# Kernel tuning notes

Hardware: AMD Instinct MI355X
Metric: run time of the kernel (lower is better)

## Reference

```python
import jax, jax.numpy as jnp
import numpy as np

HEADS = 4
DIM_HEAD = 32
DIM = 64
NUM_MEM = 4


def _rmsnorm(t, g, dim):
    # F.normalize(x, dim=1) * g * sqrt(dim)  (eps=1e-12 like torch)
    n = jnp.sqrt(jnp.sum(t * t, axis=1, keepdims=True))
    return t / jnp.maximum(n, 1e-12) * g * (dim ** 0.5)


def setup_inputs() -> dict:
    key = jax.random.key(0)
    ks = jax.random.split(key, 7)
    b, c, H, W, D = 2, DIM, 48, 48, 48
    hidden = HEADS * DIM_HEAD
    x = jax.random.normal(ks[0], (b, c, H, W, D), dtype=jnp.float32)
    g_in = jnp.ones((1, c, 1, 1, 1), dtype=jnp.float32)
    w_qkv = jax.random.normal(ks[1], (hidden * 3, c), dtype=jnp.float32) * 0.02  # 1x1 conv3d
    mem_kv = jax.random.normal(ks[2], (2, HEADS, DIM_HEAD, NUM_MEM), dtype=jnp.float32)
    w_out = jax.random.normal(ks[3], (c, hidden), dtype=jnp.float32) * 0.02
    b_out = jnp.zeros((c,), dtype=jnp.float32)
    g_out = jnp.ones((1, c, 1, 1, 1), dtype=jnp.float32)
    return {"x": x, "g_in": g_in, "w_qkv": w_qkv, "mem_kv": mem_kv,
            "w_out": w_out, "b_out": b_out, "g_out": g_out}


def reference(x, g_in, w_qkv, mem_kv, w_out, b_out, g_out):
    b, c, H, W, D = x.shape
    n = H * W * D
    scale = DIM_HEAD ** -0.5
    xn = _rmsnorm(x, g_in, c)
    # 1x1 conv3d == channel matmul
    qkv = jnp.einsum('oc,bcxyz->boxyz', w_qkv, xn)
    q, k, v = jnp.split(qkv, 3, axis=1)
    to_heads = lambda t: t.reshape(b, HEADS, DIM_HEAD, n)
    q, k, v = map(to_heads, (q, k, v))
    mk = jnp.broadcast_to(mem_kv[0], (b, HEADS, DIM_HEAD, NUM_MEM))
    mv = jnp.broadcast_to(mem_kv[1], (b, HEADS, DIM_HEAD, NUM_MEM))
    k = jnp.concatenate([mk, k], axis=-1)
    v = jnp.concatenate([mv, v], axis=-1)
    q = jax.nn.softmax(q, axis=-2) * scale  # softmax over head dim
    k = jax.nn.softmax(k, axis=-1)          # softmax over sequence dim
    context = jnp.einsum('bhdn,bhen->bhde', k, v)   # [b,h,d,e]
    out = jnp.einsum('bhde,bhdn->bhen', context, q)  # [b,h,e,n]
    out = out.reshape(b, HEADS * DIM_HEAD, H, W, D)
    out = jnp.einsum('oc,bcxyz->boxyz', w_out, out) + b_out[None, :, None, None, None]
    return _rmsnorm(out, g_out, c)
```

## Files before the change

### kernel.cpp

```cpp
#include <hip/hip_runtime.h>
#include <math.h>

#define NPOS 110592

typedef float f32x4 __attribute__((ext_vector_type(4)));
typedef short bf16x8 __attribute__((ext_vector_type(8)));
typedef unsigned u32;
typedef u32 u32x2 __attribute__((ext_vector_type(2)));
typedef u32 u32x4 __attribute__((ext_vector_type(4)));

#define MFMA __builtin_amdgcn_mfma_f32_16x16x32_bf16

__device__ __forceinline__ short f2bf(float f) {
    u32 u = __builtin_bit_cast(u32, f);
    u += 0x7fffu + ((u >> 16) & 1u);
    return (short)(u >> 16);
}
__device__ __forceinline__ u32 pack2(float a, float b) {
    return (u32)(unsigned short)f2bf(a) | ((u32)(unsigned short)f2bf(b) << 16);
}

union FragU { u32 w[4]; bf16x8 v; };
__device__ __forceinline__ bf16x8 padfrag(u32 a, u32 b) {
    FragU f; f.w[0] = a; f.w[1] = b; f.w[2] = 0u; f.w[3] = 0u; return f.v;
}

__global__ __launch_bounds__(256) void la_prep(const float* __restrict__ wqkv,
                                               const float* __restrict__ g_in,
                                               const float* __restrict__ wout,
                                               short* __restrict__ wqkv_bf,
                                               short* __restrict__ wout_bf)
{
    int i = blockIdx.x * 256 + threadIdx.x;
    if (i < 24576) wqkv_bf[i] = f2bf(wqkv[i] * g_in[i & 63]);
    if (i < 8192)  wout_bf[i] = f2bf(wout[i]);
}

__global__ __launch_bounds__(256, 3) void la_p01(
    const float* __restrict__ x, const short* __restrict__ wkv,
    short* __restrict__ xnT, float* __restrict__ partials)
{
    __shared__ __align__(16) char smem[34816];
    char* xnz = smem;
    float (*lctx)[2][32][33] = (float (*)[2][32][33])smem;
    float (*lz)[2][32]       = (float (*)[2][32])(smem + 33792);

    const int tid = threadIdx.x, lane = tid & 63, wid = tid >> 6;
    const int g = lane >> 4, m = lane & 15;
    const int blk = blockIdx.x;
    const int batch = blk / 432;
    const int pb = (blk % 432) * 256;

    const float* base = x + (size_t)batch * 64 * NPOS + pb + tid;
    float xv[64]; float ss = 0.f;
#pragma unroll
    for (int c = 0; c < 64; ++c) { float t = base[(size_t)c * NPOS]; xv[c] = t; ss += t * t; }
    float rn = 8.0f / fmaxf(sqrtf(ss), 1e-12f);

    char* row = xnz + tid * 128;
#pragma unroll
    for (int ch = 0; ch < 8; ++ch) {
        u32x4 w;
        w.x = pack2(xv[ch*8+0] * rn, xv[ch*8+1] * rn);
        w.y = pack2(xv[ch*8+2] * rn, xv[ch*8+3] * rn);
        w.z = pack2(xv[ch*8+4] * rn, xv[ch*8+5] * rn);
        w.w = pack2(xv[ch*8+6] * rn, xv[ch*8+7] * rn);
        *(u32x4*)(row + ((ch ^ (tid & 7)) << 4)) = w;
    }
    __syncthreads();

    char* dst = (char*)xnT + ((size_t)batch * NPOS + pb) * 128;
#pragma unroll
    for (int i = 0; i < 8; ++i) {
        int u = i * 256 + tid;
        int r = u >> 3, cl = u & 7;
        u32x4 w = *(const u32x4*)(xnz + r * 128 + ((cl ^ (r & 7)) << 4));
        *(u32x4*)(dst + (size_t)u * 16) = w;
    }

    const int cg = wid >> 1, hbase = (wid & 1) * 2;

    bf16x8 wkA[2][2][2], wvA[2][2][2];
#pragma unroll
    for (int hh = 0; hh < 2; ++hh) {
#pragma unroll
        for (int dt = 0; dt < 2; ++dt) {
            const short* wr = wkv + (size_t)(128 + (hbase + hh) * 32 + dt * 16 + m) * 64 + g * 8;
            wkA[hh][dt][0] = *(const bf16x8*)wr;
            wkA[hh][dt][1] = *(const bf16x8*)(wr + 32);
        }
#pragma unroll
        for (int et = 0; et < 2; ++et) {
            const short* wr = wkv + (size_t)(256 + (hbase + hh) * 32 + et * 16 + m) * 64 + g * 8;
            wvA[hh][et][0] = *(const bf16x8*)wr;
            wvA[hh][et][1] = *(const bf16x8*)(wr + 32);
        }
    }

    f32x4 acc[2][2][2];
#pragma unroll
    for (int hh = 0; hh < 2; ++hh)
#pragma unroll
        for (int dt = 0; dt < 2; ++dt)
#pragma unroll
            for (int et = 0; et < 2; ++et) acc[hh][dt][et] = (f32x4){0.f, 0.f, 0.f, 0.f};
    float zacc[2][2] = {{0.f, 0.f}, {0.f, 0.f}};

#pragma unroll 1
    for (int ic = 0; ic < 4; ++ic) {
        bf16x8 af[2][2];
#pragma unroll
        for (int mt = 0; mt < 2; ++mt)
#pragma unroll
            for (int kf = 0; kf < 2; ++kf) {
                int rowi = cg * 128 + ic * 32 + mt * 16 + m;
                af[mt][kf] = *(const bf16x8*)(xnz + rowi * 128 + (((kf*4+g) ^ (rowi & 7)) << 4));
            }
#pragma unroll
        for (int hh = 0; hh < 2; ++hh) {
            u32 ek[2][2][2], vv[2][2][2];
#pragma unroll
            for (int dt = 0; dt < 2; ++dt) {
#pragma unroll
                for (int mt = 0; mt < 2; ++mt) {
                    f32x4 a = {0.f, 0.f, 0.f, 0.f};
                    a = MFMA(af[mt][0], wkA[hh][dt][0], a, 0, 0, 0);
                    a = MFMA(af[mt][1], wkA[hh][dt][1], a, 0, 0, 0);
                    float e0 = __expf(a[0]), e1 = __expf(a[1]);
                    float e2 = __expf(a[2]), e3 = __expf(a[3]);
                    zacc[hh][dt] += (e0 + e1) + (e2 + e3);
                    ek[dt][mt][0] = pack2(e0, e1);
                    ek[dt][mt][1] = pack2(e2, e3);
                }
            }
#pragma unroll
            for (int et = 0; et < 2; ++et) {
#pragma unroll
                for (int mt = 0; mt < 2; ++mt) {
                    f32x4 a = {0.f, 0.f, 0.f, 0.f};
                    a = MFMA(af[mt][0], wvA[hh][et][0], a, 0, 0, 0);
                    a = MFMA(af[mt][1], wvA[hh][et][1], a, 0, 0, 0);
                    vv[et][mt][0] = pack2(a[0], a[1]);
                    vv[et][mt][1] = pack2(a[2], a[3]);
                }
            }
#pragma unroll
            for (int dt = 0; dt < 2; ++dt)
#pragma unroll
                for (int et = 0; et < 2; ++et)
#pragma unroll
                    for (int mt = 0; mt < 2; ++mt)
                        acc[hh][dt][et] = MFMA(padfrag(ek[dt][mt][0], ek[dt][mt][1]),
                                               padfrag(vv[et][mt][0], vv[et][mt][1]),
                                               acc[hh][dt][et], 0, 0, 0);
        }
    }

    __syncthreads();
#pragma unroll
    for (int hh = 0; hh < 2; ++hh) {
#pragma unroll
        for (int dt = 0; dt < 2; ++dt) {
#pragma unroll
            for (int et = 0; et < 2; ++et)
#pragma unroll
                for (int r4 = 0; r4 < 4; ++r4)
                    lctx[wid][hh][dt * 16 + g * 4 + r4][et * 16 + m] = acc[hh][dt][et][r4];
            float z = zacc[hh][dt];
            z += __shfl_xor(z, 16);
            z += __shfl_xor(z, 32);
            if (g == 0) lz[wid][hh][dt * 16 + m] = z;
        }
    }
    __syncthreads();

    float* P = partials + (size_t)blk * 4224;
    for (int i = tid; i < 4096; i += 256) {
        int h = i >> 10, de = i & 1023, d = de >> 5, e = de & 31;
        int w0 = h >> 1, hh2 = h & 1;
        P[i] = lctx[w0][hh2][d][e] + lctx[w0 + 2][hh2][d][e];
    }
    if (tid < 128) {
        int h = tid >> 5, d = tid & 31;
        P[4096 + tid] = lz[h >> 1][h & 1][d] + lz[(h >> 1) + 2][h & 1][d];
    }
}

__global__ __launch_bounds__(256) void la_ctxt_a(const float* __restrict__ partials,
                                                 float* __restrict__ part2)
{
    int t = blockIdx.x * 256 + threadIdx.x;
    int b = t / 67584;
    int rem = t % 67584;
    int grp = rem / 4224;
    int i = rem % 4224;
    const float* P = partials + ((size_t)(b * 432 + grp * 27)) * 4224 + i;
    float s = 0.f;
#pragma unroll 3
    for (int j = 0; j < 27; ++j) s += P[(size_t)j * 4224];
    part2[((size_t)(b * 16 + grp)) * 4224 + i] = s;
}

__global__ __launch_bounds__(256) void la_ctxt_b(const float* __restrict__ part2,
                                                 const float* __restrict__ mem_kv,
                                                 u32* __restrict__ ctxA)
{
    __shared__ float ctxN[32][33];
    const int tid = threadIdx.x;
    const int b = blockIdx.x >> 2, h = blockIdx.x & 3;
    const float* P = part2 + (size_t)b * 16 * 4224;
#pragma unroll
    for (int u = 0; u < 4; ++u) {
        int de = tid * 4 + u;
        int d = de >> 5, e = de & 31;
        float S = 0.f, Z = 0.f;
#pragma unroll 4
        for (int grp = 0; grp < 16; ++grp) {
            S += P[(size_t)grp * 4224 + h * 1024 + de];
            Z += P[(size_t)grp * 4224 + 4096 + h * 32 + d];
        }
        const float* mk = mem_kv + (h * 32 + d) * 4;
        const float* mv = mem_kv + 512 + (h * 32 + e) * 4;
#pragma unroll
        for (int mm = 0; mm < 4; ++mm) {
            float ekv = __expf(mk[mm]);
            S += ekv * mv[mm];
            Z += ekv;
        }
        ctxN[d][e] = S / Z;
    }
    __syncthreads();
#pragma unroll
    for (int k = 0; k < 2; ++k) {
        int j = tid * 2 + k;
        int q = j & 1, lanej = (j >> 1) & 63, dt = (j >> 7) & 1, et = (j >> 8) & 1;
        int gg = lanej >> 4, mm = lanej & 15;
        int d0 = dt * 16 + gg * 4 + 2 * q, e = et * 16 + mm;
        ctxA[(size_t)(b * 4 + h) * 512 + j] = pack2(ctxN[d0][e], ctxN[d0 + 1][e]);
    }
}

__global__ __launch_bounds__(256, 3) void la_pass2(
    const short* __restrict__ xnT, const short* __restrict__ wq,
    const u32* __restrict__ ctxA, const short* __restrict__ wout,
    const float* __restrict__ b_out, const float* __restrict__ g_out,
    float* __restrict__ out)
{
    const int tid = threadIdx.x, lane = tid & 63, wid = tid >> 6;
    const int g = lane >> 4, m = lane & 15;
    const int blk = blockIdx.x;
    const int batch = blk / 432;
    const int task = (blk % 432) * 4 + wid;
    const int posbase = task * 64;

    const short* xp = xnT + ((size_t)batch * NPOS + posbase) * 64;
    bf16x8 af[4][2];
#pragma unroll
    for (int mt = 0; mt < 4; ++mt)
#pragma unroll
        for (int kf = 0; kf < 2; ++kf)
            af[mt][kf] = *(const bf16x8*)(xp + (mt * 16 + m) * 64 + kf * 32 + g * 8);

    f32x4 oacc[4][4];
#pragma unroll
    for (int ct = 0; ct < 4; ++ct)
#pragma unroll
        for (int mt = 0; mt < 4; ++mt) oacc[ct][mt] = (f32x4){0.f, 0.f, 0.f, 0.f};

    const float scale = 0.17677669529663687f;
    const u32* cab = ctxA + (size_t)batch * 4 * 512;

#pragma unroll 1
    for (int h = 0; h < 4; ++h) {
        u32 eqB[2][4][2];
        float dpart[4] = {0.f, 0.f, 0.f, 0.f};
#pragma unroll
        for (int dt = 0; dt < 2; ++dt) {
            const short* wr = wq + (size_t)(h * 32 + dt * 16 + m) * 64 + g * 8;
            bf16x8 a0 = *(const bf16x8*)wr;
            bf16x8 a1 = *(const bf16x8*)(wr + 32);
#pragma unroll
            for (int mt = 0; mt < 4; ++mt) {
                f32x4 a = {0.f, 0.f, 0.f, 0.f};
                a = MFMA(a0, af[mt][0], a, 0, 0, 0);
                a = MFMA(a1, af[mt][1], a, 0, 0, 0);
                float e0 = __expf(a[0]), e1 = __expf(a[1]);
                float e2 = __expf(a[2]), e3 = __expf(a[3]);
                dpart[mt] += (e0 + e1) + (e2 + e3);
                eqB[dt][mt][0] = pack2(e0, e1);
                eqB[dt][mt][1] = pack2(e2, e3);
            }
        }
        float inv[4];
#pragma unroll
        for (int mt = 0; mt < 4; ++mt) {
            float dn = dpart[mt];
            dn += __shfl_xor(dn, 16);
            dn += __shfl_xor(dn, 32);
            inv[mt] = scale / dn;
        }
        u32 hidB[2][4][2];
#pragma unroll
        for (int et = 0; et < 2; ++et) {
            u32x2 c0 = *(const u32x2*)(cab + h * 512 + et * 256 + 0 * 128 + lane * 2);
            u32x2 c1 = *(const u32x2*)(cab + h * 512 + et * 256 + 1 * 128 + lane * 2);
#pragma unroll
            for (int mt = 0; mt < 4; ++mt) {
                f32x4 hh2 = {0.f, 0.f, 0.f, 0.f};
                hh2 = MFMA(padfrag(c0.x, c0.y), padfrag(eqB[0][mt][0], eqB[0][mt][1]), hh2, 0, 0, 0);
                hh2 = MFMA(padfrag(c1.x, c1.y), padfrag(eqB[1][mt][0], eqB[1][mt][1]), hh2, 0, 0, 0);
                hidB[et][mt][0] = pack2(hh2[0] * inv[mt], hh2[1] * inv[mt]);
                hidB[et][mt][1] = pack2(hh2[2] * inv[mt], hh2[3] * inv[mt]);
            }
        }
#pragma unroll
        for (int ct = 0; ct < 4; ++ct)
#pragma unroll
            for (int et = 0; et < 2; ++et) {
                u32x2 wv = *(const u32x2*)(wout + (size_t)(ct * 16 + m) * 128
                                           + h * 32 + et * 16 + g * 4);
                bf16x8 wfr = padfrag(wv.x, wv.y);
#pragma unroll
                for (int mt = 0; mt < 4; ++mt)
                    oacc[ct][mt] = MFMA(wfr, padfrag(hidB[et][mt][0], hidB[et][mt][1]),
                                        oacc[ct][mt], 0, 0, 0);
            }
    }

    float bo[4][4], go[4][4];
#pragma unroll
    for (int ct = 0; ct < 4; ++ct)
#pragma unroll
        for (int r = 0; r < 4; ++r) {
            int c = ct * 16 + g * 4 + r;
            bo[ct][r] = b_out[c];
            go[ct][r] = g_out[c];
        }
    float* ob = out + (size_t)batch * 64 * NPOS;
#pragma unroll
    for (int mt = 0; mt < 4; ++mt) {
        float vv[4][4]; float s2 = 0.f;
#pragma unroll
        for (int ct = 0; ct < 4; ++ct)
#pragma unroll
            for (int r = 0; r < 4; ++r) {
                float v = oacc[ct][mt][r] + bo[ct][r];
                vv[ct][r] = v;
                s2 += v * v;
            }
        s2 += __shfl_xor(s2, 16);
        s2 += __shfl_xor(s2, 32);
        float rn2 = 8.0f / fmaxf(sqrtf(s2), 1e-12f);
        int pn = posbase + mt * 16 + m;
#pragma unroll
        for (int ct = 0; ct < 4; ++ct)
#pragma unroll
            for (int r = 0; r < 4; ++r)
                ob[(size_t)(ct * 16 + g * 4 + r) * NPOS + pn] = vv[ct][r] * rn2 * go[ct][r];
    }
}

extern "C" void kernel_launch(void* const* d_in, const int* in_sizes, int n_in,
                              void* d_out, int out_size, void* d_ws, size_t ws_size,
                              hipStream_t stream) {
    const float* x      = (const float*)d_in[0];
    const float* g_in   = (const float*)d_in[1];
    const float* w_qkv  = (const float*)d_in[2];
    const float* mem_kv = (const float*)d_in[3];
    const float* w_out  = (const float*)d_in[4];
    const float* b_out  = (const float*)d_in[5];
    const float* g_out  = (const float*)d_in[6];
    float* out = (float*)d_out;

    char* ws = (char*)d_ws;
    short* xnT     = (short*)(ws);
    float* part2   = (float*)(ws + 28311552);
    short* wqkv_bf = (short*)(ws + 28852224);
    short* wout_bf = (short*)(ws + 28901376);
    u32*   ctxA    = (u32*)  (ws + 28917760);

    float* partials = (float*)d_out;

    la_prep<<<96, 256, 0, stream>>>(w_qkv, g_in, w_out, wqkv_bf, wout_bf);
    la_p01<<<864, 256, 0, stream>>>(x, wqkv_bf, xnT, partials);
    la_ctxt_a<<<528, 256, 0, stream>>>(partials, part2);
    la_ctxt_b<<<8, 256, 0, stream>>>(part2, mem_kv, ctxA);
    la_pass2<<<864, 256, 0, stream>>>(xnT, wqkv_bf, ctxA, wout_bf, b_out, g_out, out);
}
```

Before: 96.32 us.

## Fold per-head context into output projection weights and move xnT store later

Result: no change. 98.02 us (+1.8%).

```diff
diff --git a/kernel.cpp b/kernel.cpp
--- a/kernel.cpp
+++ b/kernel.cpp
@@ -27,13 +27,10 @@
 
 __global__ __launch_bounds__(256) void la_prep(const float* __restrict__ wqkv,
                                                const float* __restrict__ g_in,
-                                               const float* __restrict__ wout,
-                                               short* __restrict__ wqkv_bf,
-                                               short* __restrict__ wout_bf)
+                                               short* __restrict__ wqkv_bf)
 {
     int i = blockIdx.x * 256 + threadIdx.x;
     if (i < 24576) wqkv_bf[i] = f2bf(wqkv[i] * g_in[i & 63]);
-    if (i < 8192)  wout_bf[i] = f2bf(wout[i]);
 }
 
 __global__ __launch_bounds__(256, 3) void la_p01(
@@ -68,15 +65,6 @@
         *(u32x4*)(row + ((ch ^ (tid & 7)) << 4)) = w;
     }
     __syncthreads();
-
-    char* dst = (char*)xnT + ((size_t)batch * NPOS + pb) * 128;
-#pragma unroll
-    for (int i = 0; i < 8; ++i) {
-        int u = i * 256 + tid;
-        int r = u >> 3, cl = u & 7;
-        u32x4 w = *(const u32x4*)(xnz + r * 128 + ((cl ^ (r & 7)) << 4));
-        *(u32x4*)(dst + (size_t)u * 16) = w;
-    }
 
     const int cg = wid >> 1, hbase = (wid & 1) * 2;
 
@@ -156,6 +144,15 @@
         }
     }
 
+    char* dst = (char*)xnT + ((size_t)batch * NPOS + pb) * 128;
+#pragma unroll
+    for (int i = 0; i < 8; ++i) {
+        int u = i * 256 + tid;
+        int r = u >> 3, cl = u & 7;
+        u32x4 w = *(const u32x4*)(xnz + r * 128 + ((cl ^ (r & 7)) << 4));
+        *(u32x4*)(dst + (size_t)u * 16) = w;
+    }
+
     __syncthreads();
 #pragma unroll
     for (int hh = 0; hh < 2; ++hh) {
@@ -203,7 +200,8 @@
 
 __global__ __launch_bounds__(256) void la_ctxt_b(const float* __restrict__ part2,
                                                  const float* __restrict__ mem_kv,
-                                                 u32* __restrict__ ctxA)
+                                                 const float* __restrict__ wout_f,
+                                                 short* __restrict__ W2bf)
 {
     __shared__ float ctxN[32][33];
     const int tid = threadIdx.x;
@@ -231,20 +229,21 @@
     }
     __syncthreads();
 #pragma unroll
-    for (int k = 0; k < 2; ++k) {
-        int j = tid * 2 + k;
-        int q = j & 1, lanej = (j >> 1) & 63, dt = (j >> 7) & 1, et = (j >> 8) & 1;
-        int gg = lanej >> 4, mm = lanej & 15;
-        int d0 = dt * 16 + gg * 4 + 2 * q, e = et * 16 + mm;
-        ctxA[(size_t)(b * 4 + h) * 512 + j] = pack2(ctxN[d0][e], ctxN[d0 + 1][e]);
-    }
-}
-
-__global__ __launch_bounds__(256, 3) void la_pass2(
+    for (int u = 0; u < 8; ++u) {
+        int idx = u * 256 + tid;
+        int c = idx >> 5, d = idx & 31;
+        const float* wr = wout_f + c * 128 + h * 32;
+        float s = 0.f;
+#pragma unroll
+        for (int e = 0; e < 32; ++e) s += wr[e] * ctxN[d][e];
+        W2bf[(size_t)(b * 64 + c) * 128 + h * 32 + d] = f2bf(s);
+    }
+}
+
+__global__ __launch_bounds__(256, 2) void la_pass2(
     const short* __restrict__ xnT, const short* __restrict__ wq,
-    const u32* __restrict__ ctxA, const short* __restrict__ wout,
-    const float* __restrict__ b_out, const float* __restrict__ g_out,
-    float* __restrict__ out)
+    const short* __restrict__ W2, const float* __restrict__ b_out,
+    const float* __restrict__ g_out, float* __restrict__ out)
 {
     const int tid = threadIdx.x, lane = tid & 63, wid = tid >> 6;
     const int g = lane >> 4, m = lane & 15;
@@ -268,12 +267,11 @@
         for (int mt = 0; mt < 4; ++mt) oacc[ct][mt] = (f32x4){0.f, 0.f, 0.f, 0.f};
 
     const float scale = 0.17677669529663687f;
-    const u32* cab = ctxA + (size_t)batch * 4 * 512;
+    const short* w2b = W2 + (size_t)batch * 8192;
 
 #pragma unroll 1
     for (int h = 0; h < 4; ++h) {
-        u32 eqB[2][4][2];
-        float dpart[4] = {0.f, 0.f, 0.f, 0.f};
+        f32x4 aa[2][4];
 #pragma unroll
         for (int dt = 0; dt < 2; ++dt) {
             const short* wr = wq + (size_t)(h * 32 + dt * 16 + m) * 64 + g * 8;
@@ -284,45 +282,38 @@
                 f32x4 a = {0.f, 0.f, 0.f, 0.f};
                 a = MFMA(a0, af[mt][0], a, 0, 0, 0);
                 a = MFMA(a1, af[mt][1], a, 0, 0, 0);
-                float e0 = __expf(a[0]), e1 = __expf(a[1]);
-                float e2 = __expf(a[2]), e3 = __expf(a[3]);
-                dpart[mt] += (e0 + e1) + (e2 + e3);
-                eqB[dt][mt][0] = pack2(e0, e1);
-                eqB[dt][mt][1] = pack2(e2, e3);
+                aa[dt][mt][0] = __expf(a[0]);
+                aa[dt][mt][1] = __expf(a[1]);
+                aa[dt][mt][2] = __expf(a[2]);
+                aa[dt][mt][3] = __expf(a[3]);
             }
         }
         float inv[4];
 #pragma unroll
         for (int mt = 0; mt < 4; ++mt) {
-            float dn = dpart[mt];
+            float dn = (aa[0][mt][0] + aa[0][mt][1]) + (aa[0][mt][2] + aa[0][mt][3])
+                     + (aa[1][mt][0] + aa[1][mt][1]) + (aa[1][mt][2] + aa[1][mt][3]);
             dn += __shfl_xor(dn, 16);
             dn += __shfl_xor(dn, 32);
             inv[mt] = scale / dn;
         }
-        u32 hidB[2][4][2];
-#pragma unroll
-        for (int et = 0; et < 2; ++et) {
-            u32x2 c0 = *(const u32x2*)(cab + h * 512 + et * 256 + 0 * 128 + lane * 2);
-            u32x2 c1 = *(const u32x2*)(cab + h * 512 + et * 256 + 1 * 128 + lane * 2);
+        u32 eqn[2][4][2];
+#pragma unroll
+        for (int dt = 0; dt < 2; ++dt)
 #pragma unroll
             for (int mt = 0; mt < 4; ++mt) {
-                f32x4 hh2 = {0.f, 0.f, 0.f, 0.f};
-                hh2 = MFMA(padfrag(c0.x, c0.y), padfrag(eqB[0][mt][0], eqB[0][mt][1]), hh2, 0, 0, 0);
-                hh2 = MFMA(padfrag(c1.x, c1.y), padfrag(eqB[1][mt][0], eqB[1][mt][1]), hh2, 0, 0, 0);
-                hidB[et][mt][0] = pack2(hh2[0] * inv[mt], hh2[1] * inv[mt]);
-                hidB[et][mt][1] = pack2(hh2[2] * inv[mt], hh2[3] * inv[mt]);
-            }
-        }
+                eqn[dt][mt][0] = pack2(aa[dt][mt][0] * inv[mt], aa[dt][mt][1] * inv[mt]);
+                eqn[dt][mt][1] = pack2(aa[dt][mt][2] * inv[mt], aa[dt][mt][3] * inv[mt]);
+            }
 #pragma unroll
         for (int ct = 0; ct < 4; ++ct)
 #pragma unroll
-            for (int et = 0; et < 2; ++et) {
-                u32x2 wv = *(const u32x2*)(wout + (size_t)(ct * 16 + m) * 128
-                                           + h * 32 + et * 16 + g * 4);
+            for (int dt = 0; dt < 2; ++dt) {
+                u32x2 wv = *(const u32x2*)(w2b + (ct * 16 + m) * 128 + h * 32 + dt * 16 + g * 4);
                 bf16x8 wfr = padfrag(wv.x, wv.y);
 #pragma unroll
                 for (int mt = 0; mt < 4; ++mt)
-                    oacc[ct][mt] = MFMA(wfr, padfrag(hidB[et][mt][0], hidB[et][mt][1]),
+                    oacc[ct][mt] = MFMA(wfr, padfrag(eqn[dt][mt][0], eqn[dt][mt][1]),
                                         oacc[ct][mt], 0, 0, 0);
             }
     }
@@ -376,14 +367,13 @@
     short* xnT     = (short*)(ws);
     float* part2   = (float*)(ws + 28311552);
     short* wqkv_bf = (short*)(ws + 28852224);
-    short* wout_bf = (short*)(ws + 28901376);
-    u32*   ctxA    = (u32*)  (ws + 28917760);
+    short* W2bf    = (short*)(ws + 28901376);
 
     float* partials = (float*)d_out;
 
-    la_prep<<<96, 256, 0, stream>>>(w_qkv, g_in, w_out, wqkv_bf, wout_bf);
+    la_prep<<<96, 256, 0, stream>>>(w_qkv, g_in, wqkv_bf);
     la_p01<<<864, 256, 0, stream>>>(x, wqkv_bf, xnT, partials);
     la_ctxt_a<<<528, 256, 0, stream>>>(partials, part2);
-    la_ctxt_b<<<8, 256, 0, stream>>>(part2, mem_kv, ctxA);
-    la_pass2<<<864, 256, 0, stream>>>(xnT, wqkv_bf, ctxA, wout_bf, b_out, g_out, out);
-}
+    la_ctxt_b<<<8, 256, 0, stream>>>(part2, mem_kv, w_out, W2bf);
+    la_pass2<<<864, 256, 0, stream>>>(xnT, wqkv_bf, W2bf, b_out, g_out, out);
+}
```
